# Optimization experiments

Measured on AMD Instinct MI355X. Metric: run time of the kernel, lower is better.

Reference implementation:

```python
import jax, jax.numpy as jnp
import numpy as np

N, DEG, NUM_TYPES = 50000, 16, 2
E = N * DEG
EPS = 1e-15


def setup_inputs() -> dict:
    rng = np.random.default_rng(0)
    pos = jnp.asarray((rng.normal(size=(N, 3)) * 2.0).astype(np.float32))
    # fixed-degree graph: node i owns edges [i*DEG, (i+1)*DEG)
    src = np.repeat(np.arange(N, dtype=np.int64), DEG)
    dst = (src + rng.integers(1, N, size=E)) % N  # no self-edges
    edge_index = jnp.asarray(np.stack([src, dst]).astype(np.int32))
    # triplets = all unordered pairs of edges sharing a source node (edge_ij < edge_ik),
    # exactly what radius(source_nodes, source_nodes, r=0) + mask produces in torch.
    a, b = np.triu_indices(DEG, k=1)  # a < b -> edge_ij < edge_ik within a node block
    base = (np.arange(N, dtype=np.int64) * DEG)[:, None]
    trip_ij = jnp.asarray((base + a[None, :]).reshape(-1).astype(np.int32))
    trip_ik = jnp.asarray((base + b[None, :]).reshape(-1).astype(np.int32))
    atom_types = jnp.asarray(rng.integers(0, NUM_TYPES, size=N).astype(np.int32))
    interaction_map = jnp.asarray(np.array([[0, 1], [1, 2]], dtype=np.int32))
    batch = jnp.zeros((N,), dtype=jnp.int32)  # single structure
    # real Si-like Tersoff constants, 3 pair types
    vals = {
        'A': [1830.8, 1500.0, 1200.0], 'B': [471.18, 400.0, 350.0],
        'lambda1': [2.4799, 2.6, 2.8], 'lambda2': [1.7322, 1.8, 1.9],
        'lambda3': [1.7322, 1.5, 1.3], 'beta': [1.1e-6, 2e-6, 3e-6],
        'n': [0.78734, 0.8, 0.9], 'gamma': [1.0, 1.0, 1.0],
        'c': [100390.0, 90000.0, 80000.0], 'd': [16.217, 15.0, 14.0],
    }
    logs = {f'log_{k}': jnp.log(jnp.asarray(v, dtype=jnp.float32)) for k, v in vals.items()}
    return dict(
        pos=pos, **logs,
        E_ref=jnp.asarray([-4.63, -3.5], dtype=jnp.float32),
        h_values=jnp.asarray([-0.59825, -0.5, -0.4], dtype=jnp.float32),
        R_cutoff=jnp.asarray([2.85, 3.0, 3.1], dtype=jnp.float32),
        D_width=jnp.asarray([0.15, 0.2, 0.2], dtype=jnp.float32),
        edge_index=edge_index, trip_ij=trip_ij, trip_ik=trip_ik,
        atom_types=atom_types, interaction_map=interaction_map, batch=batch,
    )


def _cutoff(r, R, D):
    arg = jnp.pi * (r - R + D) / (2.0 * D + EPS)
    trans = 0.5 - 0.5 * jnp.sin(arg)
    return jnp.where(r < R - D, 1.0, jnp.where(r < R + D, trans, 0.0))


def _angular(cos_t, gamma, c, d, h):
    c2, d2 = c * c, d * d
    hm = h - cos_t
    return gamma * (1.0 + c2 / (d2 + EPS) - c2 / (d2 + hm * hm + EPS))


def reference(pos, log_A, log_B, log_lambda1, log_lambda2, log_lambda3,
              log_beta, log_n, log_gamma, log_c, log_d, E_ref,
              h_values, R_cutoff, D_width,
              edge_index, trip_ij, trip_ik, atom_types, interaction_map, batch):
    src, dst = edge_index[0], edge_index[1]
    epi = interaction_map[atom_types[src], atom_types[dst]]          # [E] pair-type per edge
    A = jnp.exp(log_A)[epi]; B = jnp.exp(log_B)[epi]
    lam1 = jnp.exp(log_lambda1)[epi]; lam2 = jnp.exp(log_lambda2)[epi]
    vec = pos[dst] - pos[src]                                        # [E,3]
    r = jnp.linalg.norm(vec, axis=1)                                 # [E]
    repulsive = A * jnp.exp(-lam1 * r)
    attractive = -B * jnp.exp(-lam2 * r)
    # ---- three-body bond order (training_phase == 2 path) ----
    vij, vik = vec[trip_ij], vec[trip_ik]                            # [T,3]
    rij, rik = r[trip_ij], r[trip_ik]
    cos_t = jnp.clip(jnp.sum(vij * vik, axis=1) / (rij * rik + EPS), -1.0, 1.0)
    ti = atom_types[src[trip_ij]]
    tj = atom_types[dst[trip_ij]]
    tk = atom_types[dst[trip_ik]]
    pik = interaction_map[ti, tk]
    pij = interaction_map[ti, tj]
    gamma = jnp.exp(log_gamma); c = jnp.exp(log_c); d = jnp.exp(log_d)
    lam3 = jnp.exp(log_lambda3)
    ang = _angular(cos_t, gamma[pik], c[pik], d[pik], h_values[pik])
    fc_ik = _cutoff(rik, R_cutoff[pik], D_width[pik])
    fc_ij = _cutoff(rij, R_cutoff[pij], D_width[pij])
    z_ij = fc_ik * ang * jnp.exp(jnp.minimum(lam3[pik] * (rij - rik), 35.0))
    z_ik = fc_ij * ang * jnp.exp(jnp.minimum(lam3[pij] * (rik - rij), 35.0))
    zeta = jnp.zeros_like(r).at[trip_ij].add(z_ij).at[trip_ik].add(z_ik)
    n_e = jnp.exp(log_n)[epi]; beta_e = jnp.exp(log_beta)[epi]
    bond_order = (1.0 + (beta_e * zeta) ** n_e) ** (-1.0 / (2.0 * n_e + EPS))
    # ---- pair energy + per-atom reduction ----
    fc = _cutoff(r, R_cutoff[epi], D_width[epi])
    pair_e = fc * (repulsive + bond_order * attractive)
    atomic = jax.ops.segment_sum(0.5 * pair_e, src, num_segments=N) + E_ref[atom_types]
    total = jax.ops.segment_sum(atomic, batch, num_segments=1)       # [1]
    return total
```

## Files before the change

### kernel.cpp

```cpp
#include <hip/hip_runtime.h>
#include <math.h>

#ifndef M_PI
#define M_PI 3.14159265358979323846
#endif

#define DEG 16
#define NPB 16
#define THREADS (DEG * NPB)
#define TILES_PER_BLOCK 2

__global__ __launch_bounds__(THREADS) void tersoff_main(
    const float* __restrict__ pos,
    const float* __restrict__ log_A,  const float* __restrict__ log_B,
    const float* __restrict__ log_l1, const float* __restrict__ log_l2,
    const float* __restrict__ log_l3, const float* __restrict__ log_beta,
    const float* __restrict__ log_n,  const float* __restrict__ log_gamma,
    const float* __restrict__ log_c,  const float* __restrict__ log_d,
    const float* __restrict__ E_ref,  const float* __restrict__ h_vals,
    const float* __restrict__ R_cut,  const float* __restrict__ D_wid,
    const int*  __restrict__ edge_dst,
    const int*  __restrict__ atom_types,
    const int*  __restrict__ imap,
    float* __restrict__ partials, int nAtoms, int nTiles)
{
    __shared__ float PT[3][16];
    __shared__ int   IM[4];
    __shared__ float ER[2];
    __shared__ float4 ED[NPB][DEG + 1][3];
    __shared__ float WS[THREADS / 64];

    if (threadIdx.x < 3) {
        int t = threadIdx.x;
        float A  = expf(log_A[t]);   float B  = expf(log_B[t]);
        float l1 = expf(log_l1[t]);  float l2 = expf(log_l2[t]);
        float l3 = expf(log_l3[t]);  float be = expf(log_beta[t]);
        float nn = expf(log_n[t]);   float ga = expf(log_gamma[t]);
        float c  = expf(log_c[t]);   float d  = expf(log_d[t]);
        float c2 = c * c, d2 = d * d;
        float R  = R_cut[t], D = D_wid[t];
        PT[t][0] = A;   PT[t][1] = B;
        PT[t][2] = l1;  PT[t][3] = l2;
        PT[t][4] = l3;  PT[t][5] = be;
        PT[t][6] = nn;  PT[t][7] = -1.0f / (2.0f * nn);
        PT[t][8] = h_vals[t];
        PT[t][9] = ga * (1.0f + c2 / d2);
        PT[t][10] = ga * c2;
        PT[t][11] = d2;
        PT[t][12] = R - D;
        PT[t][13] = R + D;
        PT[t][14] = (float)M_PI / (2.0f * D);
    }
    if (threadIdx.x >= 64 && threadIdx.x < 68) IM[threadIdx.x - 64] = imap[threadIdx.x - 64];
    if (threadIdx.x >= 68 && threadIdx.x < 70) ER[threadIdx.x - 68] = E_ref[threadIdx.x - 68];
    __syncthreads();

    int nl   = threadIdx.x >> 4;
    int e    = threadIdx.x & (DEG - 1);
    int lane = threadIdx.x & 63;

    float acc = 0.0f;

    for (int tile = blockIdx.x; tile < nTiles; tile += gridDim.x) {
        int node = tile * NPB + nl;
        bool valid = (node < nAtoms);
        int nc = valid ? node : 0;

        int dst = edge_dst[nc * DEG + e];
        int ti  = atom_types[nc];
        int tj  = atom_types[dst];
        int p   = IM[ti * 2 + tj];

        float vx = pos[3 * dst]     - pos[3 * nc];
        float vy = pos[3 * dst + 1] - pos[3 * nc + 1];
        float vz = pos[3 * dst + 2] - pos[3 * nc + 2];
        float r2 = vx * vx + vy * vy + vz * vz;
        float inv_r = __builtin_amdgcn_rsqf(r2);
        float r = r2 * inv_r;

        float RmD = PT[p][12], RpD = PT[p][13], piD = PT[p][14];
        float fc;
        if (r < RmD)      fc = 1.0f;
        else if (r < RpD) fc = 0.5f - 0.5f * __sinf(piD * (r - RmD));
        else              fc = 0.0f;
        if (!valid) fc = 0.0f;

        float h  = PT[p][8], g1 = PT[p][9], gc2 = PT[p][10], d2 = PT[p][11];
        float ux = vx * inv_r, uy = vy * inv_r, uz = vz * inv_r;

        unsigned long long bal = __ballot(fc > 0.0f);
        unsigned gm  = (unsigned)((bal >> (lane & 48)) & 0xFFFFull);
        int nact = __popc(gm);
        int rank = __popc(gm & ((1u << (lane & 15)) - 1u));
        if (fc > 0.0f) {
            ED[nl][rank][0] = make_float4(ux, uy, uz, r);
            ED[nl][rank][1] = make_float4(fc, PT[p][4], h, g1);
            ED[nl][rank][2] = make_float4(gc2, d2, 0.0f, 0.0f);
        }
        if (valid && e == 0) acc += ER[ti];
        __syncthreads();

        if (fc > 0.0f) {
            float zeta = 0.0f;
            for (int s = 0; s < nact; ++s) {
                if (s == rank) continue;
                float4 fa = ED[nl][s][0];
                float4 fb = ED[nl][s][1];
                float4 fx = ED[nl][s][2];
                float ct = ux * fa.x + uy * fa.y + uz * fa.z;
                ct = fminf(fmaxf(ct, -1.0f), 1.0f);
                bool mine = (s < rank);
                float hh  = mine ? h   : fb.z;
                float G1  = mine ? g1  : fb.w;
                float GC2 = mine ? gc2 : fx.x;
                float D2  = mine ? d2  : fx.y;
                float hm  = hh - ct;
                float ang = G1 - GC2 * __builtin_amdgcn_rcpf(D2 + hm * hm);
                float ex  = __expf(fminf(fb.y * (r - fa.w), 35.0f));
                zeta += fb.x * ang * ex;
            }
            float be  = PT[p][5], nn = PT[p][6], m2n = PT[p][7];
            float xx  = __powf(be * zeta, nn);
            float bo  = __powf(1.0f + xx, m2n);
            float rep =  PT[p][0] * __expf(-PT[p][2] * r);
            float att = -PT[p][1] * __expf(-PT[p][3] * r);
            acc += 0.5f * fc * (rep + bo * att);
        }
        __syncthreads();
    }

    for (int o = 32; o > 0; o >>= 1) acc += __shfl_down(acc, o, 64);
    if ((threadIdx.x & 63) == 0) WS[threadIdx.x >> 6] = acc;
    __syncthreads();
    if (threadIdx.x == 0) {
        float s = 0.0f;
        #pragma unroll
        for (int w = 0; w < THREADS / 64; ++w) s += WS[w];
        partials[blockIdx.x] = s;
    }
}

__global__ __launch_bounds__(256) void reduce_kernel(
    const float* __restrict__ in, int n, float* __restrict__ out)
{
    float acc = 0.0f;
    for (int i = threadIdx.x; i < n; i += 256) acc += in[i];
    for (int o = 32; o > 0; o >>= 1) acc += __shfl_down(acc, o, 64);
    __shared__ float WS[4];
    if ((threadIdx.x & 63) == 0) WS[threadIdx.x >> 6] = acc;
    __syncthreads();
    if (threadIdx.x == 0) out[0] = WS[0] + WS[1] + WS[2] + WS[3];
}

extern "C" void kernel_launch(void* const* d_in, const int* in_sizes, int n_in,
                              void* d_out, int out_size, void* d_ws, size_t ws_size,
                              hipStream_t stream) {
    const float* pos      = (const float*)d_in[0];
    const float* log_A    = (const float*)d_in[1];
    const float* log_B    = (const float*)d_in[2];
    const float* log_l1   = (const float*)d_in[3];
    const float* log_l2   = (const float*)d_in[4];
    const float* log_l3   = (const float*)d_in[5];
    const float* log_beta = (const float*)d_in[6];
    const float* log_n    = (const float*)d_in[7];
    const float* log_gam  = (const float*)d_in[8];
    const float* log_c    = (const float*)d_in[9];
    const float* log_d    = (const float*)d_in[10];
    const float* E_ref    = (const float*)d_in[11];
    const float* h_vals   = (const float*)d_in[12];
    const float* R_cut    = (const float*)d_in[13];
    const float* D_wid    = (const float*)d_in[14];
    const int*   edge_idx = (const int*)d_in[15];
    const int*   atypes   = (const int*)d_in[18];
    const int*   imap     = (const int*)d_in[19];

    int nAtoms = in_sizes[0] / 3;
    int E      = in_sizes[15] / 2;
    const int* edge_dst = edge_idx + E;

    int nTiles = (nAtoms + NPB - 1) / NPB;
    int grid   = (nTiles + TILES_PER_BLOCK - 1) / TILES_PER_BLOCK;

    float* partials = (float*)d_ws;

    tersoff_main<<<grid, THREADS, 0, stream>>>(
        pos, log_A, log_B, log_l1, log_l2, log_l3, log_beta, log_n,
        log_gam, log_c, log_d, E_ref, h_vals, R_cut, D_wid,
        edge_dst, atypes, imap, partials, nAtoms, nTiles);

    reduce_kernel<<<1, 256, 0, stream>>>(partials, grid, (float*)d_out);
}
```

Measured before the change: 25.71 us.

## Pack positions with types, compress per-edge LDS record, drop block barriers

A new pre-kernel packs xyz and atom type into a float4 per atom, so the main kernel does one vector gather per endpoint instead of separate position and type loads. The per-edge shared record shrinks from three float4s to one (raw vector plus a sign-encoded cutoff and type); the partner's distance and parameters are recomputed inside the triplet loop. The __syncthreads calls are removed because each node's 16 edges sit in one wavefront, and the triplet loop is unrolled by two with masking. The cost is an extra kernel launch and more per-pair ALU work (an extra rsqrt and selects). Correctness now relies on implicit intra-wave LDS ordering.

```diff
diff --git a/kernel.cpp b/kernel.cpp
--- a/kernel.cpp
+++ b/kernel.cpp
@@ -10,8 +10,20 @@
 #define THREADS (DEG * NPB)
 #define TILES_PER_BLOCK 2
 
+#define RSQ(x) __builtin_amdgcn_rsqf(x)
+#define RCP(x) __builtin_amdgcn_rcpf(x)
+
+__global__ __launch_bounds__(256) void pack_kernel(
+    const float* __restrict__ pos, const int* __restrict__ atom_types,
+    float4* __restrict__ pos4, int nAtoms)
+{
+    for (int i = blockIdx.x * 256 + threadIdx.x; i < nAtoms; i += gridDim.x * 256)
+        pos4[i] = make_float4(pos[3 * i], pos[3 * i + 1], pos[3 * i + 2],
+                              __int_as_float(atom_types[i]));
+}
+
 __global__ __launch_bounds__(THREADS) void tersoff_main(
-    const float* __restrict__ pos,
+    const float4* __restrict__ pos4,
     const float* __restrict__ log_A,  const float* __restrict__ log_B,
     const float* __restrict__ log_l1, const float* __restrict__ log_l2,
     const float* __restrict__ log_l3, const float* __restrict__ log_beta,
@@ -20,14 +32,11 @@
     const float* __restrict__ E_ref,  const float* __restrict__ h_vals,
     const float* __restrict__ R_cut,  const float* __restrict__ D_wid,
     const int*  __restrict__ edge_dst,
-    const int*  __restrict__ atom_types,
     const int*  __restrict__ imap,
     float* __restrict__ partials, int nAtoms, int nTiles)
 {
-    __shared__ float PT[3][16];
-    __shared__ int   IM[4];
-    __shared__ float ER[2];
-    __shared__ float4 ED[NPB][DEG + 1][3];
+    __shared__ float4 PT4[3][4];
+    __shared__ float4 ED[NPB][DEG + 1];
     __shared__ float WS[THREADS / 64];
 
     if (threadIdx.x < 3) {
@@ -39,21 +48,15 @@
         float c  = expf(log_c[t]);   float d  = expf(log_d[t]);
         float c2 = c * c, d2 = d * d;
         float R  = R_cut[t], D = D_wid[t];
-        PT[t][0] = A;   PT[t][1] = B;
-        PT[t][2] = l1;  PT[t][3] = l2;
-        PT[t][4] = l3;  PT[t][5] = be;
-        PT[t][6] = nn;  PT[t][7] = -1.0f / (2.0f * nn);
-        PT[t][8] = h_vals[t];
-        PT[t][9] = ga * (1.0f + c2 / d2);
-        PT[t][10] = ga * c2;
-        PT[t][11] = d2;
-        PT[t][12] = R - D;
-        PT[t][13] = R + D;
-        PT[t][14] = (float)M_PI / (2.0f * D);
+        PT4[t][0] = make_float4(l3, h_vals[t], ga * (1.0f + c2 / d2), ga * c2);
+        PT4[t][1] = make_float4(d2, R - D, R + D, (float)M_PI / (2.0f * D));
+        PT4[t][2] = make_float4(A, B, l1, l2);
+        PT4[t][3] = make_float4(be, nn, -1.0f / (2.0f * nn), 0.0f);
     }
-    if (threadIdx.x >= 64 && threadIdx.x < 68) IM[threadIdx.x - 64] = imap[threadIdx.x - 64];
-    if (threadIdx.x >= 68 && threadIdx.x < 70) ER[threadIdx.x - 68] = E_ref[threadIdx.x - 68];
     __syncthreads();
+
+    int im00 = imap[0], im01 = imap[1], im10 = imap[2], im11 = imap[3];
+    float er0 = E_ref[0], er1 = E_ref[1];
 
     int nl   = threadIdx.x >> 4;
     int e    = threadIdx.x & (DEG - 1);
@@ -67,66 +70,98 @@
         int nc = valid ? node : 0;
 
         int dst = edge_dst[nc * DEG + e];
-        int ti  = atom_types[nc];
-        int tj  = atom_types[dst];
-        int p   = IM[ti * 2 + tj];
-
-        float vx = pos[3 * dst]     - pos[3 * nc];
-        float vy = pos[3 * dst + 1] - pos[3 * nc + 1];
-        float vz = pos[3 * dst + 2] - pos[3 * nc + 2];
+        float4 P0 = pos4[nc];
+        float4 P1 = pos4[dst];
+        int ti = __float_as_int(P0.w);
+        bool tjb = (__float_as_int(P1.w) != 0);
+
+        int p0 = ti ? im10 : im00;
+        int p1 = ti ? im11 : im01;
+        float4 ZA0 = PT4[p0][0], ZB0 = PT4[p0][1];
+        float4 ZA1 = PT4[p1][0], ZB1 = PT4[p1][1];
+
+        float vx = P1.x - P0.x, vy = P1.y - P0.y, vz = P1.z - P0.z;
         float r2 = vx * vx + vy * vy + vz * vz;
-        float inv_r = __builtin_amdgcn_rsqf(r2);
+        float inv_r = RSQ(r2);
         float r = r2 * inv_r;
 
-        float RmD = PT[p][12], RpD = PT[p][13], piD = PT[p][14];
+        float RmD = tjb ? ZB1.y : ZB0.y;
+        float RpD = tjb ? ZB1.z : ZB0.z;
+        float piD = tjb ? ZB1.w : ZB0.w;
         float fc;
         if (r < RmD)      fc = 1.0f;
         else if (r < RpD) fc = 0.5f - 0.5f * __sinf(piD * (r - RmD));
         else              fc = 0.0f;
         if (!valid) fc = 0.0f;
 
-        float h  = PT[p][8], g1 = PT[p][9], gc2 = PT[p][10], d2 = PT[p][11];
-        float ux = vx * inv_r, uy = vy * inv_r, uz = vz * inv_r;
+        float h_o   = tjb ? ZA1.y : ZA0.y;
+        float g1_o  = tjb ? ZA1.z : ZA0.z;
+        float gc2_o = tjb ? ZA1.w : ZA0.w;
+        float d2_o  = tjb ? ZB1.x : ZB0.x;
 
         unsigned long long bal = __ballot(fc > 0.0f);
         unsigned gm  = (unsigned)((bal >> (lane & 48)) & 0xFFFFull);
         int nact = __popc(gm);
         int rank = __popc(gm & ((1u << (lane & 15)) - 1u));
-        if (fc > 0.0f) {
-            ED[nl][rank][0] = make_float4(ux, uy, uz, r);
-            ED[nl][rank][1] = make_float4(fc, PT[p][4], h, g1);
-            ED[nl][rank][2] = make_float4(gc2, d2, 0.0f, 0.0f);
-        }
-        if (valid && e == 0) acc += ER[ti];
-        __syncthreads();
+        if (fc > 0.0f)
+            ED[nl][rank] = make_float4(vx, vy, vz, tjb ? -fc : fc);
+
+        if (valid && e == 0) acc += ti ? er1 : er0;
 
         if (fc > 0.0f) {
             float zeta = 0.0f;
-            for (int s = 0; s < nact; ++s) {
-                if (s == rank) continue;
-                float4 fa = ED[nl][s][0];
-                float4 fb = ED[nl][s][1];
-                float4 fx = ED[nl][s][2];
-                float ct = ux * fa.x + uy * fa.y + uz * fa.z;
-                ct = fminf(fmaxf(ct, -1.0f), 1.0f);
-                bool mine = (s < rank);
-                float hh  = mine ? h   : fb.z;
-                float G1  = mine ? g1  : fb.w;
-                float GC2 = mine ? gc2 : fx.x;
-                float D2  = mine ? d2  : fx.y;
-                float hm  = hh - ct;
-                float ang = G1 - GC2 * __builtin_amdgcn_rcpf(D2 + hm * hm);
-                float ex  = __expf(fminf(fb.y * (r - fa.w), 35.0f));
-                zeta += fb.x * ang * ex;
+            for (int s = 0; s < nact; s += 2) {
+                float4 qa = ED[nl][s];
+                float4 qb = ED[nl][s + 1];
+                {
+                    bool  tjk = (qa.w < 0.0f);
+                    float fck = fabsf(qa.w);
+                    float r2k = qa.x * qa.x + qa.y * qa.y + qa.z * qa.z;
+                    float irk = RSQ(r2k);
+                    float rk  = r2k * irk;
+                    float ct  = (vx * qa.x + vy * qa.y + vz * qa.z) * inv_r * irk;
+                    ct = fminf(fmaxf(ct, -1.0f), 1.0f);
+                    bool mine = (s < rank);
+                    float lam3k = tjk ? ZA1.x : ZA0.x;
+                    float hh  = mine ? h_o   : (tjk ? ZA1.y : ZA0.y);
+                    float G1  = mine ? g1_o  : (tjk ? ZA1.z : ZA0.z);
+                    float GC2 = mine ? gc2_o : (tjk ? ZA1.w : ZA0.w);
+                    float D2  = mine ? d2_o  : (tjk ? ZB1.x : ZB0.x);
+                    float hm  = hh - ct;
+                    float ang = G1 - GC2 * RCP(D2 + hm * hm);
+                    float ex  = __expf(fminf(lam3k * (r - rk), 35.0f));
+                    float term = fck * ang * ex;
+                    zeta += (s == rank) ? 0.0f : term;
+                }
+                {
+                    int sb = s + 1;
+                    bool  tjk = (qb.w < 0.0f);
+                    float fck = fabsf(qb.w);
+                    float r2k = qb.x * qb.x + qb.y * qb.y + qb.z * qb.z;
+                    float irk = RSQ(r2k);
+                    float rk  = r2k * irk;
+                    float ct  = (vx * qb.x + vy * qb.y + vz * qb.z) * inv_r * irk;
+                    ct = fminf(fmaxf(ct, -1.0f), 1.0f);
+                    bool mine = (sb < rank);
+                    float lam3k = tjk ? ZA1.x : ZA0.x;
+                    float hh  = mine ? h_o   : (tjk ? ZA1.y : ZA0.y);
+                    float G1  = mine ? g1_o  : (tjk ? ZA1.z : ZA0.z);
+                    float GC2 = mine ? gc2_o : (tjk ? ZA1.w : ZA0.w);
+                    float D2  = mine ? d2_o  : (tjk ? ZB1.x : ZB0.x);
+                    float hm  = hh - ct;
+                    float ang = G1 - GC2 * RCP(D2 + hm * hm);
+                    float ex  = __expf(fminf(lam3k * (r - rk), 35.0f));
+                    float term = fck * ang * ex;
+                    zeta += (sb >= nact || sb == rank) ? 0.0f : term;
+                }
             }
-            float be  = PT[p][5], nn = PT[p][6], m2n = PT[p][7];
-            float xx  = __powf(be * zeta, nn);
-            float bo  = __powf(1.0f + xx, m2n);
-            float rep =  PT[p][0] * __expf(-PT[p][2] * r);
-            float att = -PT[p][1] * __expf(-PT[p][3] * r);
-            acc += 0.5f * fc * (rep + bo * att);
+            int pb = tjb ? p1 : p0;
+            float4 C  = PT4[pb][2];
+            float4 Dd = PT4[pb][3];
+            float xx = __powf(Dd.x * zeta, Dd.y);
+            float bo = __powf(1.0f + xx, Dd.z);
+            acc += 0.5f * fc * (C.x * __expf(-C.z * r) - bo * C.y * __expf(-C.w * r));
         }
-        __syncthreads();
     }
 
     for (int o = 32; o > 0; o >>= 1) acc += __shfl_down(acc, o, 64);
@@ -181,12 +216,16 @@
     int nTiles = (nAtoms + NPB - 1) / NPB;
     int grid   = (nTiles + TILES_PER_BLOCK - 1) / TILES_PER_BLOCK;
 
-    float* partials = (float*)d_ws;
-
+    char* ws = (char*)d_ws;
+    size_t pos4_off = ((size_t)grid * 4 + 255) & ~(size_t)255;
+    float*  partials = (float*)ws;
+    float4* pos4     = (float4*)(ws + pos4_off);
+
+    int pblk = (nAtoms + 255) / 256;
+    pack_kernel<<<pblk, 256, 0, stream>>>(pos, atypes, pos4, nAtoms);
     tersoff_main<<<grid, THREADS, 0, stream>>>(
-        pos, log_A, log_B, log_l1, log_l2, log_l3, log_beta, log_n,
+        pos4, log_A, log_B, log_l1, log_l2, log_l3, log_beta, log_n,
         log_gam, log_c, log_d, E_ref, h_vals, R_cut, D_wid,
-        edge_dst, atypes, imap, partials, nAtoms, nTiles);
-
+        edge_dst, imap, partials, nAtoms, nTiles);
     reduce_kernel<<<1, 256, 0, stream>>>(partials, grid, (float*)d_out);
 }
```

Result: slower. 32.26 us (+25.5%).

## Pack positions and atom types into float4 and prefetch both tiles' gathers upfront

Applied to the files above, without the earlier changes.

A new pre-pass kernel packs each atom's xyz position and its atom type into a single float4, so every neighbour gather becomes one 16-byte load instead of three scalar position loads plus a type load. The main kernel drops the tile loop and processes exactly two tiles per block, issuing the edge and position loads for both tiles before any compute so their global-memory latency overlaps. In exchange it adds an extra kernel launch and a workspace buffer. It also hard-codes two tiles per block and assumes atom types are 0 or 1.

```diff
diff --git a/kernel.cpp b/kernel.cpp
--- a/kernel.cpp
+++ b/kernel.cpp
@@ -8,10 +8,18 @@
 #define DEG 16
 #define NPB 16
 #define THREADS (DEG * NPB)
-#define TILES_PER_BLOCK 2
+
+__global__ __launch_bounds__(256) void pack_kernel(
+    const float* __restrict__ pos, const int* __restrict__ atom_types,
+    float4* __restrict__ pos4, int nAtoms)
+{
+    for (int i = blockIdx.x * 256 + threadIdx.x; i < nAtoms; i += gridDim.x * 256)
+        pos4[i] = make_float4(pos[3 * i], pos[3 * i + 1], pos[3 * i + 2],
+                              __int_as_float(atom_types[i]));
+}
 
 __global__ __launch_bounds__(THREADS) void tersoff_main(
-    const float* __restrict__ pos,
+    const float4* __restrict__ pos4,
     const float* __restrict__ log_A,  const float* __restrict__ log_B,
     const float* __restrict__ log_l1, const float* __restrict__ log_l2,
     const float* __restrict__ log_l3, const float* __restrict__ log_beta,
@@ -20,7 +28,6 @@
     const float* __restrict__ E_ref,  const float* __restrict__ h_vals,
     const float* __restrict__ R_cut,  const float* __restrict__ D_wid,
     const int*  __restrict__ edge_dst,
-    const int*  __restrict__ atom_types,
     const int*  __restrict__ imap,
     float* __restrict__ partials, int nAtoms, int nTiles)
 {
@@ -59,75 +66,77 @@
     int e    = threadIdx.x & (DEG - 1);
     int lane = threadIdx.x & 63;
 
+    int t0 = blockIdx.x;
+    int t1 = blockIdx.x + gridDim.x;
+    int node0 = t0 * NPB + nl;  bool v0 = (node0 < nAtoms);  int nc0 = v0 ? node0 : 0;
+    int node1 = t1 * NPB + nl;  bool v1 = (node1 < nAtoms);  int nc1 = v1 ? node1 : 0;
+    int dst0 = edge_dst[nc0 * DEG + e];
+    int dst1 = edge_dst[nc1 * DEG + e];
+    float4 P00 = pos4[nc0];   float4 P10 = pos4[dst0];
+    float4 P01 = pos4[nc1];   float4 P11 = pos4[dst1];
+
     float acc = 0.0f;
 
-    for (int tile = blockIdx.x; tile < nTiles; tile += gridDim.x) {
-        int node = tile * NPB + nl;
-        bool valid = (node < nAtoms);
-        int nc = valid ? node : 0;
-
-        int dst = edge_dst[nc * DEG + e];
-        int ti  = atom_types[nc];
-        int tj  = atom_types[dst];
-        int p   = IM[ti * 2 + tj];
-
-        float vx = pos[3 * dst]     - pos[3 * nc];
-        float vy = pos[3 * dst + 1] - pos[3 * nc + 1];
-        float vz = pos[3 * dst + 2] - pos[3 * nc + 2];
-        float r2 = vx * vx + vy * vy + vz * vz;
-        float inv_r = __builtin_amdgcn_rsqf(r2);
-        float r = r2 * inv_r;
-
-        float RmD = PT[p][12], RpD = PT[p][13], piD = PT[p][14];
-        float fc;
-        if (r < RmD)      fc = 1.0f;
-        else if (r < RpD) fc = 0.5f - 0.5f * __sinf(piD * (r - RmD));
-        else              fc = 0.0f;
-        if (!valid) fc = 0.0f;
-
-        float h  = PT[p][8], g1 = PT[p][9], gc2 = PT[p][10], d2 = PT[p][11];
-        float ux = vx * inv_r, uy = vy * inv_r, uz = vz * inv_r;
-
-        unsigned long long bal = __ballot(fc > 0.0f);
-        unsigned gm  = (unsigned)((bal >> (lane & 48)) & 0xFFFFull);
-        int nact = __popc(gm);
-        int rank = __popc(gm & ((1u << (lane & 15)) - 1u));
-        if (fc > 0.0f) {
-            ED[nl][rank][0] = make_float4(ux, uy, uz, r);
-            ED[nl][rank][1] = make_float4(fc, PT[p][4], h, g1);
-            ED[nl][rank][2] = make_float4(gc2, d2, 0.0f, 0.0f);
-        }
-        if (valid && e == 0) acc += ER[ti];
-        __syncthreads();
-
-        if (fc > 0.0f) {
-            float zeta = 0.0f;
-            for (int s = 0; s < nact; ++s) {
-                if (s == rank) continue;
-                float4 fa = ED[nl][s][0];
-                float4 fb = ED[nl][s][1];
-                float4 fx = ED[nl][s][2];
-                float ct = ux * fa.x + uy * fa.y + uz * fa.z;
-                ct = fminf(fmaxf(ct, -1.0f), 1.0f);
-                bool mine = (s < rank);
-                float hh  = mine ? h   : fb.z;
-                float G1  = mine ? g1  : fb.w;
-                float GC2 = mine ? gc2 : fx.x;
-                float D2  = mine ? d2  : fx.y;
-                float hm  = hh - ct;
-                float ang = G1 - GC2 * __builtin_amdgcn_rcpf(D2 + hm * hm);
-                float ex  = __expf(fminf(fb.y * (r - fa.w), 35.0f));
-                zeta += fb.x * ang * ex;
-            }
-            float be  = PT[p][5], nn = PT[p][6], m2n = PT[p][7];
-            float xx  = __powf(be * zeta, nn);
-            float bo  = __powf(1.0f + xx, m2n);
-            float rep =  PT[p][0] * __expf(-PT[p][2] * r);
-            float att = -PT[p][1] * __expf(-PT[p][3] * r);
-            acc += 0.5f * fc * (rep + bo * att);
-        }
-        __syncthreads();
+#define PROCESS_TILE(P0v, P1v, validv)                                         \
+    {                                                                          \
+        int ti = __float_as_int(P0v.w);                                        \
+        int tj = __float_as_int(P1v.w);                                        \
+        int p  = IM[ti * 2 + tj];                                              \
+        float vx = P1v.x - P0v.x, vy = P1v.y - P0v.y, vz = P1v.z - P0v.z;      \
+        float r2 = vx * vx + vy * vy + vz * vz;                                \
+        float inv_r = __builtin_amdgcn_rsqf(r2);                               \
+        float r = r2 * inv_r;                                                  \
+        float RmD = PT[p][12], RpD = PT[p][13], piD = PT[p][14];               \
+        float fc;                                                              \
+        if (r < RmD)      fc = 1.0f;                                           \
+        else if (r < RpD) fc = 0.5f - 0.5f * __sinf(piD * (r - RmD));          \
+        else              fc = 0.0f;                                           \
+        if (!(validv)) fc = 0.0f;                                              \
+        float h  = PT[p][8], g1 = PT[p][9], gc2 = PT[p][10], d2 = PT[p][11];   \
+        float ux = vx * inv_r, uy = vy * inv_r, uz = vz * inv_r;               \
+        unsigned long long bal = __ballot(fc > 0.0f);                          \
+        unsigned gm  = (unsigned)((bal >> (lane & 48)) & 0xFFFFull);           \
+        int nact = __popc(gm);                                                 \
+        int rank = __popc(gm & ((1u << (lane & 15)) - 1u));                    \
+        if (fc > 0.0f) {                                                       \
+            ED[nl][rank][0] = make_float4(ux, uy, uz, r);                      \
+            ED[nl][rank][1] = make_float4(fc, PT[p][4], h, g1);                \
+            ED[nl][rank][2] = make_float4(gc2, d2, 0.0f, 0.0f);                \
+        }                                                                      \
+        if ((validv) && e == 0) acc += ti ? ER[1] : ER[0];                     \
+        __syncthreads();                                                       \
+        if (fc > 0.0f) {                                                       \
+            float zeta = 0.0f;                                                 \
+            for (int s = 0; s < nact; ++s) {                                   \
+                if (s == rank) continue;                                       \
+                float4 fa = ED[nl][s][0];                                      \
+                float4 fb = ED[nl][s][1];                                      \
+                float4 fx = ED[nl][s][2];                                      \
+                float ct = ux * fa.x + uy * fa.y + uz * fa.z;                  \
+                ct = fminf(fmaxf(ct, -1.0f), 1.0f);                            \
+                bool mine = (s < rank);                                        \
+                float hh  = mine ? h   : fb.z;                                 \
+                float G1  = mine ? g1  : fb.w;                                 \
+                float GC2 = mine ? gc2 : fx.x;                                 \
+                float D2  = mine ? d2  : fx.y;                                 \
+                float hm  = hh - ct;                                           \
+                float ang = G1 - GC2 * __builtin_amdgcn_rcpf(D2 + hm * hm);    \
+                float ex  = __expf(fminf(fb.y * (r - fa.w), 35.0f));           \
+                zeta += fb.x * ang * ex;                                       \
+            }                                                                  \
+            float be  = PT[p][5], nn = PT[p][6], m2n = PT[p][7];               \
+            float xx  = __powf(be * zeta, nn);                                 \
+            float bo  = __powf(1.0f + xx, m2n);                                \
+            float rep =  PT[p][0] * __expf(-PT[p][2] * r);                     \
+            float att = -PT[p][1] * __expf(-PT[p][3] * r);                     \
+            acc += 0.5f * fc * (rep + bo * att);                               \
+        }                                                                      \
+        __syncthreads();                                                       \
     }
+
+    PROCESS_TILE(P00, P10, v0)
+    PROCESS_TILE(P01, P11, v1)
+#undef PROCESS_TILE
 
     for (int o = 32; o > 0; o >>= 1) acc += __shfl_down(acc, o, 64);
     if ((threadIdx.x & 63) == 0) WS[threadIdx.x >> 6] = acc;
@@ -179,14 +188,18 @@
     const int* edge_dst = edge_idx + E;
 
     int nTiles = (nAtoms + NPB - 1) / NPB;
-    int grid   = (nTiles + TILES_PER_BLOCK - 1) / TILES_PER_BLOCK;
-
-    float* partials = (float*)d_ws;
-
+    int grid   = (nTiles + 1) / 2;
+
+    char* ws = (char*)d_ws;
+    size_t pos4_off = ((size_t)grid * 4 + 255) & ~(size_t)255;
+    float*  partials = (float*)ws;
+    float4* pos4     = (float4*)(ws + pos4_off);
+
+    int pblk = (nAtoms + 255) / 256;
+    pack_kernel<<<pblk, 256, 0, stream>>>(pos, atypes, pos4, nAtoms);
     tersoff_main<<<grid, THREADS, 0, stream>>>(
-        pos, log_A, log_B, log_l1, log_l2, log_l3, log_beta, log_n,
+        pos4, log_A, log_B, log_l1, log_l2, log_l3, log_beta, log_n,
         log_gam, log_c, log_d, E_ref, h_vals, R_cut, D_wid,
-        edge_dst, atypes, imap, partials, nAtoms, nTiles);
-
+        edge_dst, imap, partials, nAtoms, nTiles);
     reduce_kernel<<<1, 256, 0, stream>>>(partials, grid, (float*)d_out);
 }
```

New measurement: 31.20 us. +21.4%, slower.
